# Kernel tuning notes

Measured on AMD Instinct MI355X. Metric: run time of the kernel, lower is better.

Reference implementation:

```python
import jax, jax.numpy as jnp
import numpy as np

V, D, H, L, T_MAX = 50257, 1024, 16, 12, 256
HS = D // H
B, T = 8, 256


def setup_inputs() -> dict:
    key = jax.random.key(0)
    ks = jax.random.split(key, 24)
    s = 0.02
    inp = {
        'idx': jax.random.randint(ks[0], (B, T), 0, V),
        'targets': jax.random.randint(ks[1], (B, T), 0, V),
        'tok_emb': jax.random.normal(ks[2], (V, D), jnp.float32) * s,
        'pos_emb': jax.random.normal(ks[3], (T_MAX, D), jnp.float32) * s,
        'Wq': jax.random.normal(ks[4], (L, H, D, HS), jnp.float32) / np.sqrt(D),
        'Wk': jax.random.normal(ks[5], (L, H, D, HS), jnp.float32) / np.sqrt(D),
        'Wv': jax.random.normal(ks[6], (L, H, D, HS), jnp.float32) / np.sqrt(D),
        'ln1_g': jnp.ones((L, D), jnp.float32),
        'ln1_b': jnp.zeros((L, D), jnp.float32),
        'ln2_g': jnp.ones((L, D), jnp.float32),
        'ln2_b': jnp.zeros((L, D), jnp.float32),
        'fc1_w': jax.random.normal(ks[7], (L, D, 4 * D), jnp.float32) / np.sqrt(D),
        'fc1_b': jnp.zeros((L, 4 * D), jnp.float32),
        'fc2_w': jax.random.normal(ks[8], (L, 4 * D, D), jnp.float32) / np.sqrt(4 * D),
        'fc2_b': jnp.zeros((L, D), jnp.float32),
        'lnf_g': jnp.ones((D,), jnp.float32),
        'lnf_b': jnp.zeros((D,), jnp.float32),
        'lm_w': jax.random.normal(ks[9], (D, V), jnp.float32) / np.sqrt(D),
        'lm_b': jnp.zeros((V,), jnp.float32),
    }
    return inp


def _layernorm(x, g, b, eps=1e-5):
    mu = jnp.mean(x, axis=-1, keepdims=True)
    var = jnp.var(x, axis=-1, keepdims=True)
    return (x - mu) * jax.lax.rsqrt(var + eps) * g + b


def reference(idx, targets, tok_emb, pos_emb, Wq, Wk, Wv, ln1_g, ln1_b, ln2_g, ln2_b,
              fc1_w, fc1_b, fc2_w, fc2_b, lnf_g, lnf_b, lm_w, lm_b):
    Bc, Tc = idx.shape
    x = tok_emb[idx] + pos_emb[:Tc]  # [B,T,D]
    causal = jnp.tril(jnp.ones((Tc, Tc), bool))
    scale = 1.0 / np.sqrt(HS)
    for l in range(L):
        h = _layernorm(x, ln1_g[l], ln1_b[l])
        q = jnp.einsum('btd,hds->bhts', h, Wq[l])
        k = jnp.einsum('btd,hds->bhts', h, Wk[l])
        v = jnp.einsum('btd,hds->bhts', h, Wv[l])
        scores = jnp.einsum('bhts,bhus->bhtu', q, k) * scale
        scores = jnp.where(causal, scores, -jnp.inf)
        attn = jax.nn.softmax(scores, axis=-1)
        o = jnp.einsum('bhtu,bhus->bhts', attn, v)  # [B,H,T,hs]
        o = o.transpose(0, 2, 1, 3).reshape(Bc, Tc, D)  # concat heads
        x = x + o  # no output projection in original
        h = _layernorm(x, ln2_g[l], ln2_b[l])
        ff = jax.nn.relu(h @ fc1_w[l] + fc1_b[l]) @ fc2_w[l] + fc2_b[l]
        x = x + ff
    x = _layernorm(x, lnf_g, lnf_b)
    logits = x @ lm_w + lm_b  # [B,T,V]
    logp = jax.nn.log_softmax(logits, axis=-1)
    nll = -jnp.take_along_axis(logp, targets[..., None], axis=-1)[..., 0]
    loss = jnp.mean(nll)
    return logits, loss
```

## Files before the change

kernel.cpp:

```cpp
#include <hip/hip_runtime.h>

#define T_SEQ 256
#define DMODEL 1024
#define NHEAD 16
#define HSZ 64
#define NLAYER 12
#define VOCAB 50257
#define NPAD 50304
#define FF 4096
#define MROWS 2048

using short8 = __attribute__((ext_vector_type(8))) short;
using f32x4  = __attribute__((ext_vector_type(4))) float;

__device__ __forceinline__ float bf2f(unsigned short u) {
    unsigned int x = ((unsigned int)u) << 16;
    return __builtin_bit_cast(float, x);
}
__device__ __forceinline__ unsigned short f2bf(float f) {
    unsigned int u = __builtin_bit_cast(unsigned int, f);
    unsigned int r = (u + 0x7fffu + ((u >> 16) & 1u)) >> 16;
    return (unsigned short)r;
}
__device__ __forceinline__ void async_copy16(const void* g, void* l) {
    __builtin_amdgcn_global_load_lds(
        (const __attribute__((address_space(1))) unsigned int*)g,
        (__attribute__((address_space(3))) unsigned int*)l, 16, 0, 0);
}

__device__ __forceinline__ void ln_tail(
    float4 v, const float* __restrict__ g, const float* __restrict__ b,
    int row, int tid, unsigned short* __restrict__ out)
{
    float s  = v.x + v.y + v.z + v.w;
    float ss = v.x * v.x + v.y * v.y + v.z * v.z + v.w * v.w;
    for (int o = 32; o > 0; o >>= 1) {
        s  += __shfl_down(s, o);
        ss += __shfl_down(ss, o);
    }
    __shared__ float ps[4], pss[4];
    int wave = tid >> 6, lane = tid & 63;
    if (lane == 0) { ps[wave] = s; pss[wave] = ss; }
    __syncthreads();
    float st  = ps[0] + ps[1] + ps[2] + ps[3];
    float sst = pss[0] + pss[1] + pss[2] + pss[3];
    float mu  = st * (1.0f / DMODEL);
    float var = sst * (1.0f / DMODEL) - mu * mu;
    float rstd = rsqrtf(var + 1e-5f);
    float4 gv = ((const float4*)g)[tid];
    float4 bv = ((const float4*)b)[tid];
    ushort4 o4;
    o4.x = f2bf((v.x - mu) * rstd * gv.x + bv.x);
    o4.y = f2bf((v.y - mu) * rstd * gv.y + bv.y);
    o4.z = f2bf((v.z - mu) * rstd * gv.z + bv.z);
    o4.w = f2bf((v.w - mu) * rstd * gv.w + bv.w);
    ((ushort4*)out)[(size_t)row * (DMODEL / 4) + tid] = o4;
}

__global__ __launch_bounds__(256) void embed_ln_kernel(
    const int* __restrict__ idx, const float* __restrict__ tok,
    const float* __restrict__ pos, const float* __restrict__ g,
    const float* __restrict__ b, float* __restrict__ x,
    unsigned short* __restrict__ h)
{
    int row = blockIdx.x, tid = threadIdx.x;
    int t = row & (T_SEQ - 1);
    int token = idx[row];
    float4 a = ((const float4*)(tok + (size_t)token * DMODEL))[tid];
    float4 p = ((const float4*)(pos + (size_t)t * DMODEL))[tid];
    float4 v;
    v.x = a.x + p.x; v.y = a.y + p.y; v.z = a.z + p.z; v.w = a.w + p.w;
    ((float4*)(x + (size_t)row * DMODEL))[tid] = v;
    ln_tail(v, g, b, row, tid, h);
}

__global__ __launch_bounds__(256) void ln_kernel(
    const float* __restrict__ x, const float* __restrict__ g,
    const float* __restrict__ b, unsigned short* __restrict__ out)
{
    int row = blockIdx.x, tid = threadIdx.x;
    float4 v = ((const float4*)(x + (size_t)row * DMODEL))[tid];
    ln_tail(v, g, b, row, tid, out);
}

__global__ __launch_bounds__(256) void fc2_merge_ln_kernel(
    const float* __restrict__ part, const float* __restrict__ bias,
    const float* __restrict__ g, const float* __restrict__ b,
    float* __restrict__ x, unsigned short* __restrict__ h)
{
    int row = blockIdx.x, tid = threadIdx.x;
    size_t o = (size_t)row * (DMODEL / 4) + tid;
    float4 p0 = ((const float4*)part)[o];
    float4 p1 = ((const float4*)part)[o + MROWS * (DMODEL / 4)];
    float4 bv = ((const float4*)bias)[tid];
    float4 v = ((float4*)x)[o];
    v.x += p0.x + p1.x + bv.x;
    v.y += p0.y + p1.y + bv.y;
    v.z += p0.z + p1.z + bv.z;
    v.w += p0.w + p1.w + bv.w;
    ((float4*)x)[o] = v;
    ln_tail(v, g, b, row, tid, h);
}

__global__ __launch_bounds__(256) void wtranspose_kernel(
    const float* __restrict__ in, unsigned short* __restrict__ out,
    int R, int C, int Cout, long in_l, long out_l)
{
    int lyr = blockIdx.z;
    in  += (size_t)lyr * in_l;
    out += (size_t)lyr * out_l;
    __shared__ float tile[32][33];
    int tx = threadIdx.x & 31, ty = threadIdx.x >> 5;
    int c0 = blockIdx.x * 32, r0 = blockIdx.y * 32;
    #pragma unroll
    for (int i = 0; i < 4; i++) {
        int r = r0 + ty + i * 8, c = c0 + tx;
        tile[ty + i * 8][tx] = (c < C) ? in[(size_t)r * C + c] : 0.f;
    }
    __syncthreads();
    #pragma unroll
    for (int i = 0; i < 4; i++) {
        int c = c0 + ty + i * 8, r = r0 + tx;
        if (c < Cout) out[(size_t)c * R + r] = f2bf(tile[tx][ty + i * 8]);
    }
}

__global__ __launch_bounds__(256) void qkvpack_kernel(
    const float* __restrict__ Wq, const float* __restrict__ Wk,
    const float* __restrict__ Wv, unsigned short* __restrict__ out,
    long w_l, long out_l)
{
    int z = blockIdx.z;
    int lyr = z / 48, r48 = z % 48;
    int seg = r48 >> 4, hh = r48 & 15;
    const float* W = (seg == 0 ? Wq : seg == 1 ? Wk : Wv)
                     + (size_t)lyr * w_l + (size_t)hh * DMODEL * HSZ;
    unsigned short* o = out + (size_t)lyr * out_l
                      + (size_t)(seg * 1024 + hh * 64) * DMODEL;
    __shared__ float tile[32][33];
    int tx = threadIdx.x & 31, ty = threadIdx.x >> 5;
    int d0 = blockIdx.x * 32, s0 = blockIdx.y * 32;
    #pragma unroll
    for (int i = 0; i < 4; i++)
        tile[ty + i * 8][tx] = W[(size_t)(d0 + ty + i * 8) * HSZ + s0 + tx];
    __syncthreads();
    #pragma unroll
    for (int i = 0; i < 4; i++)
        o[(size_t)(s0 + ty + i * 8) * DMODEL + d0 + tx] = f2bf(tile[tx][ty + i * 8]);
}

template<int MF, bool QKV, bool RELU, bool RES, bool CBF16>
__device__ __forceinline__ void gemm_core(
    const unsigned short* __restrict__ A, int lda,
    const unsigned short* __restrict__ Bt, int ldb,
    const float* __restrict__ bias,
    void* __restrict__ Cv, int ldc,
    const float* __restrict__ res, int ldr,
    int N, int K,
    unsigned short* __restrict__ vtout)
{
    constexpr int BM = MF * 32;
    __shared__ __align__(16) char As[2][BM * 128];
    __shared__ __align__(16) char Bs[2][128 * 128];
    int tid = threadIdx.x;
    int wave = tid >> 6, lane = tid & 63;
    int wr = wave >> 1, wc = wave & 1;
    int m0 = blockIdx.x * BM, n0 = blockIdx.y * 128;

    f32x4 acc[MF][4];
    #pragma unroll
    for (int m = 0; m < MF; m++)
        #pragma unroll
        for (int n = 0; n < 4; n++)
            acc[m][n] = (f32x4){0.f, 0.f, 0.f, 0.f};

    int ksw = (((lane & 7) ^ (lane >> 3)) << 4);
    int KT = K >> 6;

    auto stage = [&](int kt, int bi) {
        int k0 = kt << 6;
        #pragma unroll
        for (int j = 0; j < MF; j++) {
            int row = (wave * MF + j) * 8 + (lane >> 3);
            const char* src = (const char*)A + ((size_t)(m0 + row) * lda + k0) * 2 + ksw;
            async_copy16(src, As[bi] + (wave * MF + j) * 1024);
        }
        #pragma unroll
        for (int j = 0; j < 4; j++) {
            int nrow = (wave * 4 + j) * 8 + (lane >> 3);
            const char* src = (const char*)Bt + ((size_t)(n0 + nrow) * ldb + k0) * 2 + ksw;
            async_copy16(src, Bs[bi] + (wave * 4 + j) * 1024);
        }
    };

    stage(0, 0);
    __syncthreads();
    int cur = 0;
    for (int kt = 0; kt < KT; kt++) {
        if (kt + 1 < KT) stage(kt + 1, cur ^ 1);
        #pragma unroll
        for (int ks = 0; ks < 2; ks++) {
            int kb = ks * 64 + ((lane >> 4) << 4);
            short8 a[MF], b[4];
            #pragma unroll
            for (int m = 0; m < MF; m++) {
                int r = wr * (MF * 16) + m * 16 + (lane & 15);
                a[m] = *(const short8*)(const void*)(As[cur] + r * 128 + (kb ^ ((r & 7) << 4)));
            }
            #pragma unroll
            for (int n = 0; n < 4; n++) {
                int c = wc * 64 + n * 16 + (lane & 15);
                b[n] = *(const short8*)(const void*)(Bs[cur] + c * 128 + (kb ^ ((c & 7) << 4)));
            }
            #pragma unroll
            for (int m = 0; m < MF; m++)
                #pragma unroll
                for (int n = 0; n < 4; n++)
                    acc[m][n] = __builtin_amdgcn_mfma_f32_16x16x32_bf16(a[m], b[n], acc[m][n], 0, 0, 0);
        }
        __syncthreads();
        cur ^= 1;
    }
    #pragma unroll
    for (int m = 0; m < MF; m++) {
        int rowb = m0 + wr * (MF * 16) + m * 16 + ((lane >> 4) << 2);
        #pragma unroll
        for (int n = 0; n < 4; n++) {
            int col = n0 + wc * 64 + n * 16 + (lane & 15);
            if (col < N) {
                float bi = bias ? bias[col] : 0.f;
                #pragma unroll
                for (int r2 = 0; r2 < 4; r2++) {
                    float v = acc[m][n][r2] + bi;
                    if (RELU) v = fmaxf(v, 0.f);
                    int row = rowb + r2;
                    if (RES) v += res[(size_t)row * ldr + col];
                    if (QKV && col >= 2048) {
                        int hh = (col - 2048) >> 6, sdim = (col - 2048) & 63;
                        int bb = row >> 8, tt = row & 255;
                        vtout[((((size_t)bb * NHEAD + hh) * HSZ + sdim) * T_SEQ) + tt] = f2bf(v);
                    } else if (CBF16) {
                        ((unsigned short*)Cv)[(size_t)row * ldc + col] = f2bf(v);
                    } else {
                        ((float*)Cv)[(size_t)row * ldc + col] = v;
                    }
                }
            }
        }
    }
}

__global__ __launch_bounds__(256) void gemm_qkv(
    const unsigned short* __restrict__ A, const unsigned short* __restrict__ Bt,
    unsigned short* __restrict__ C, unsigned short* __restrict__ vtout)
{
    gemm_core<4, true, false, false, true>(
        A, DMODEL, Bt, DMODEL, nullptr, C, 3072, nullptr, 0, 3072, DMODEL, vtout);
}

__global__ __launch_bounds__(256) void gemm_fc1(
    const unsigned short* __restrict__ A, const unsigned short* __restrict__ Bt,
    const float* __restrict__ bias, unsigned short* __restrict__ C)
{
    gemm_core<4, false, true, false, true>(
        A, DMODEL, Bt, DMODEL, bias, C, FF, nullptr, 0, FF, DMODEL, nullptr);
}

__global__ __launch_bounds__(256) void gemm_fc2(
    const unsigned short* __restrict__ A, const unsigned short* __restrict__ Bt,
    float* __restrict__ part)
{
    int z = blockIdx.z;
    gemm_core<2, false, false, false, false>(
        A + z * 2048, FF, Bt + z * 2048, FF, nullptr,
        part + (size_t)z * MROWS * DMODEL, DMODEL, nullptr, 0,
        DMODEL, 2048, nullptr);
}

__global__ __launch_bounds__(256) void gemm_lm(
    const unsigned short* __restrict__ A, const unsigned short* __restrict__ Bt,
    const float* __restrict__ bias, float* __restrict__ C)
{
    gemm_core<4, false, false, false, false>(
        A, DMODEL, Bt, DMODEL, bias, C, VOCAB, nullptr, 0, VOCAB, DMODEL, nullptr);
}

__global__ __launch_bounds__(256) void attn_fused_kernel(
    const unsigned short* __restrict__ qkv, const unsigned short* __restrict__ vt,
    float* __restrict__ x)
{
    int qt = blockIdx.x, hh = blockIdx.y, b = blockIdx.z;
    int tid = threadIdx.x;
    int wave = tid >> 6, lane = tid & 63;
    int g = lane >> 4, q = lane & 15;

    __shared__ __align__(16) char Kb[2][8192];
    __shared__ __align__(16) char Vb[2][8192];
    __shared__ __align__(16) char Plds[4][2048];

    int qrow = b * T_SEQ + qt * 64 + wave * 16 + q;
    const char* qp = (const char*)qkv + ((size_t)qrow * 3072 + hh * HSZ) * 2;
    short8 qreg[2];
    qreg[0] = *(const short8*)(const void*)(qp + (g << 4));
    qreg[1] = *(const short8*)(const void*)(qp + 64 + (g << 4));

    char* Pw = Plds[wave];

    f32x4 oacc[4];
    #pragma unroll
    for (int f = 0; f < 4; f++) oacc[f] = (f32x4){0.f, 0.f, 0.f, 0.f};
    float m_run = -1e30f, l_run = 0.f;

    int srow = wave * 8 + (lane >> 3);
    int sbyte = ((lane & 7) << 4) ^ ((srow & 7) << 4);

    auto stage = [&](int kt, int bi) {
        #pragma unroll
        for (int c = 0; c < 2; c++) {
            int row = c * 32 + srow;
            const char* src = (const char*)qkv +
                ((size_t)(b * T_SEQ + kt * 64 + row) * 3072 + 1024 + hh * HSZ) * 2 + sbyte;
            async_copy16(src, Kb[bi] + c * 4096 + wave * 1024);
        }
        #pragma unroll
        for (int c = 0; c < 2; c++) {
            int row = c * 32 + srow;
            const char* src = (const char*)vt +
                (((size_t)(b * NHEAD + hh) * HSZ + row) * T_SEQ + kt * 64) * 2 + sbyte;
            async_copy16(src, Vb[bi] + c * 4096 + wave * 1024);
        }
    };

    stage(0, 0);
    for (int kt = 0; kt <= qt; kt++) {
        int bi = kt & 1;
        __syncthreads();
        if (kt < qt) stage(kt + 1, bi ^ 1);

        f32x4 sacc[4];
        #pragma unroll
        for (int f = 0; f < 4; f++) sacc[f] = (f32x4){0.f, 0.f, 0.f, 0.f};
        #pragma unroll
        for (int ks = 0; ks < 2; ks++) {
            int kb = ks * 64 + (g << 4);
            #pragma unroll
            for (int f = 0; f < 4; f++) {
                int u = f * 16 + q;
                short8 kf = *(const short8*)(const void*)(Kb[bi] + u * 128 + (kb ^ ((u & 7) << 4)));
                sacc[f] = __builtin_amdgcn_mfma_f32_16x16x32_bf16(kf, qreg[ks], sacc[f], 0, 0, 0);
            }
        }
        float sv[4][4];
        #pragma unroll
        for (int f = 0; f < 4; f++)
            #pragma unroll
            for (int r = 0; r < 4; r++) {
                float v = sacc[f][r] * 0.125f;
                if (kt == qt) {
                    int u_loc = f * 16 + g * 4 + r;
                    if (u_loc > wave * 16 + q) v = -1e30f;
                }
                sv[f][r] = v;
            }
        float pm = -1e30f;
        #pragma unroll
        for (int f = 0; f < 4; f++)
            #pragma unroll
            for (int r = 0; r < 4; r++) pm = fmaxf(pm, sv[f][r]);
        pm = fmaxf(pm, __shfl_xor(pm, 16));
        pm = fmaxf(pm, __shfl_xor(pm, 32));
        float mnew = fmaxf(m_run, pm);
        float corr = __expf(m_run - mnew);
        float p[4][4];
        float ls = 0.f;
        #pragma unroll
        for (int f = 0; f < 4; f++)
            #pragma unroll
            for (int r = 0; r < 4; r++) {
                p[f][r] = __expf(sv[f][r] - mnew);
                ls += p[f][r];
            }
        ls += __shfl_xor(ls, 16);
        ls += __shfl_xor(ls, 32);
        l_run = l_run * corr + ls;
        m_run = mnew;
        #pragma unroll
        for (int r = 0; r < 4; r++) {
            float cr = __shfl(corr, (lane & 48) | (g * 4 + r));
            #pragma unroll
            for (int f = 0; f < 4; f++) oacc[f][r] *= cr;
        }
        #pragma unroll
        for (int f = 0; f < 4; f++)
            #pragma unroll
            for (int rp = 0; rp < 2; rp++) {
                int ue = f * 16 + g * 4 + rp * 2;
                unsigned int pk = (unsigned int)f2bf(p[f][rp * 2])
                                | ((unsigned int)f2bf(p[f][rp * 2 + 1]) << 16);
                *(unsigned int*)(void*)(Pw + q * 128 + ((ue * 2) ^ ((q & 7) << 4))) = pk;
            }
        #pragma unroll
        for (int ks = 0; ks < 2; ks++) {
            int kb = ks * 64 + (g << 4);
            short8 pa = *(const short8*)(const void*)(Pw + q * 128 + (kb ^ ((q & 7) << 4)));
            #pragma unroll
            for (int f = 0; f < 4; f++) {
                int s = f * 16 + q;
                short8 vf = *(const short8*)(const void*)(Vb[bi] + s * 128 + (kb ^ ((s & 7) << 4)));
                oacc[f] = __builtin_amdgcn_mfma_f32_16x16x32_bf16(pa, vf, oacc[f], 0, 0, 0);
            }
        }
    }
    float inv = 1.0f / l_run;
    #pragma unroll
    for (int r = 0; r < 4; r++) {
        float ir = __shfl(inv, (lane & 48) | (g * 4 + r));
        int row_g = b * T_SEQ + qt * 64 + wave * 16 + g * 4 + r;
        #pragma unroll
        for (int f = 0; f < 4; f++) {
            size_t xi = (size_t)row_g * DMODEL + hh * HSZ + f * 16 + q;
            x[xi] += oacc[f][r] * ir;
        }
    }
}

__global__ __launch_bounds__(256) void loss1_kernel(
    const float* __restrict__ logits, const int* __restrict__ targets,
    float* __restrict__ nll)
{
    int r = blockIdx.x, tid = threadIdx.x;
    const float* row = logits + (size_t)r * VOCAB;
    const float4* row4 = (const float4*)row;
    float m = -3.4e38f, s = 0.f;
    for (int v = tid; v < VOCAB / 4; v += 256) {
        float4 x4 = row4[v];
        float lm = fmaxf(fmaxf(x4.x, x4.y), fmaxf(x4.z, x4.w));
        float nm = fmaxf(m, lm);
        s = s * __expf(m - nm) + __expf(x4.x - nm) + __expf(x4.y - nm)
          + __expf(x4.z - nm) + __expf(x4.w - nm);
        m = nm;
    }
    if (tid == 0) {
        float xv = row[VOCAB - 1];
        float nm = fmaxf(m, xv);
        s = s * __expf(m - nm) + __expf(xv - nm);
        m = nm;
    }
    __shared__ float ms[256], ssh[256];
    ms[tid] = m; ssh[tid] = s;
    __syncthreads();
    for (int o = 128; o > 0; o >>= 1) {
        if (tid < o) {
            float m1 = ms[tid], s1 = ssh[tid];
            float m2 = ms[tid + o], s2 = ssh[tid + o];
            float nm = fmaxf(m1, m2);
            ssh[tid] = s1 * __expf(m1 - nm) + s2 * __expf(m2 - nm);
            ms[tid] = nm;
        }
        __syncthreads();
    }
    if (tid == 0) nll[r] = logf(ssh[0]) + ms[0] - row[targets[r]];
}

__global__ __launch_bounds__(256) void loss2_kernel(
    const float* __restrict__ nll, float* __restrict__ out)
{
    int tid = threadIdx.x;
    float s = 0.f;
    for (int i = tid; i < MROWS; i += 256) s += nll[i];
    __shared__ float red[256];
    red[tid] = s;
    __syncthreads();
    for (int o = 128; o > 0; o >>= 1) {
        if (tid < o) red[tid] += red[tid + o];
        __syncthreads();
    }
    if (tid == 0) out[0] = red[0] * (1.0f / MROWS);
}

extern "C" void kernel_launch(void* const* d_in, const int* in_sizes, int n_in,
                              void* d_out, int out_size, void* d_ws, size_t ws_size,
                              hipStream_t stream)
{
    const int*   idx  = (const int*)d_in[0];
    const int*   tgt  = (const int*)d_in[1];
    const float* tok  = (const float*)d_in[2];
    const float* pos  = (const float*)d_in[3];
    const float* Wq   = (const float*)d_in[4];
    const float* Wk   = (const float*)d_in[5];
    const float* Wv   = (const float*)d_in[6];
    const float* ln1g = (const float*)d_in[7];
    const float* ln1b = (const float*)d_in[8];
    const float* ln2g = (const float*)d_in[9];
    const float* ln2b = (const float*)d_in[10];
    const float* fc1w = (const float*)d_in[11];
    const float* fc1b = (const float*)d_in[12];
    const float* fc2w = (const float*)d_in[13];
    const float* fc2b = (const float*)d_in[14];
    const float* lnfg = (const float*)d_in[15];
    const float* lnfb = (const float*)d_in[16];
    const float* lmw  = (const float*)d_in[17];
    const float* lmb  = (const float*)d_in[18];

    char* ws = (char*)d_ws;
    float*          x    = (float*)(ws + 0);
    unsigned short* h    = (unsigned short*)(ws + 8388608);
    unsigned short* qkv  = (unsigned short*)(ws + 12582912);
    unsigned short* vt   = (unsigned short*)(ws + 25165824);
    unsigned short* mid  = (unsigned short*)(ws + 29360128);
    float*          nll  = (float*)(ws + 46137344);
    float*          fc2p = (float*)(ws + 46145536);
    unsigned short* lmwt = (unsigned short*)(ws + 62922752);
    const size_t UP_NEED = 442769408ull;
    bool upfront = (ws_size >= UP_NEED);
    unsigned short* qkvt = (unsigned short*)(ws + 165945344);
    unsigned short* fc1t, * fc2t;
    long qkvt_l, fc1t_l, fc2t_l;
    if (upfront) {
        fc1t = (unsigned short*)(ws + 241442816);
        fc2t = (unsigned short*)(ws + 342106112);
        qkvt_l = 3072 * 1024; fc1t_l = (long)FF * 1024; fc2t_l = (long)1024 * FF;
    } else {
        fc1t = (unsigned short*)(ws + 172236800);
        fc2t = (unsigned short*)(ws + 180625408);
        qkvt_l = 0; fc1t_l = 0; fc2t_l = 0;
    }
    float* logits = (float*)d_out;
    float* lossp  = logits + (size_t)MROWS * VOCAB;

    const long WQKV_L = (long)NHEAD * DMODEL * HSZ;
    if (upfront) {
        qkvpack_kernel<<<dim3(32, 2, 48 * NLAYER), 256, 0, stream>>>(
            Wq, Wk, Wv, qkvt, WQKV_L, qkvt_l);
        wtranspose_kernel<<<dim3(128, 32, NLAYER), 256, 0, stream>>>(
            fc1w, fc1t, DMODEL, FF, FF, (long)DMODEL * FF, fc1t_l);
        wtranspose_kernel<<<dim3(32, 128, NLAYER), 256, 0, stream>>>(
            fc2w, fc2t, FF, DMODEL, DMODEL, (long)FF * DMODEL, fc2t_l);
    }
    wtranspose_kernel<<<dim3(1572, 32, 1), 256, 0, stream>>>(
        lmw, lmwt, DMODEL, VOCAB, NPAD, 0, 0);

    embed_ln_kernel<<<MROWS, 256, 0, stream>>>(idx, tok, pos, ln1g, ln1b, x, h);

    for (int l = 0; l < NLAYER; l++) {
        unsigned short* qkvt_p = qkvt + (size_t)l * qkvt_l;
        unsigned short* fc1t_p = fc1t + (size_t)l * fc1t_l;
        unsigned short* fc2t_p = fc2t + (size_t)l * fc2t_l;
        if (!upfront) {
            qkvpack_kernel<<<dim3(32, 2, 48), 256, 0, stream>>>(
                Wq + (size_t)l * WQKV_L, Wk + (size_t)l * WQKV_L,
                Wv + (size_t)l * WQKV_L, qkvt, WQKV_L, 0);
            wtranspose_kernel<<<dim3(128, 32, 1), 256, 0, stream>>>(
                fc1w + (size_t)l * DMODEL * FF, fc1t, DMODEL, FF, FF, 0, 0);
            wtranspose_kernel<<<dim3(32, 128, 1), 256, 0, stream>>>(
                fc2w + (size_t)l * FF * DMODEL, fc2t, FF, DMODEL, DMODEL, 0, 0);
        }
        gemm_qkv<<<dim3(16, 24), 256, 0, stream>>>(h, qkvt_p, qkv, vt);
        attn_fused_kernel<<<dim3(4, NHEAD, 8), 256, 0, stream>>>(qkv, vt, x);
        ln_kernel<<<MROWS, 256, 0, stream>>>(x, ln2g + l * DMODEL, ln2b + l * DMODEL, h);
        gemm_fc1<<<dim3(16, 32), 256, 0, stream>>>(h, fc1t_p, fc1b + (size_t)l * FF, mid);
        gemm_fc2<<<dim3(32, 8, 2), 256, 0, stream>>>(mid, fc2t_p, fc2p);
        const float* ng = (l < NLAYER - 1) ? ln1g + (l + 1) * DMODEL : lnfg;
        const float* nb = (l < NLAYER - 1) ? ln1b + (l + 1) * DMODEL : lnfb;
        fc2_merge_ln_kernel<<<MROWS, 256, 0, stream>>>(
            fc2p, fc2b + (size_t)l * DMODEL, ng, nb, x, h);
    }

    gemm_lm<<<dim3(16, 393), 256, 0, stream>>>(h, lmwt, lmb, logits);

    loss1_kernel<<<MROWS, 256, 0, stream>>>(logits, tgt, nll);
    loss2_kernel<<<1, 256, 0, stream>>>(nll, lossp);
}
```

Baseline: 2.257 ms.

## Drop GEMM double buffering and use 8-wave 256-row tiles for LM head

Replaces the double-buffered LDS staging in the shared GEMM core with a single buffer and two barriers per K step. This halves LDS use and may allow more blocks per CU. The LM-head GEMM now runs 512-thread blocks covering 256 rows, so each staged weight tile is reused across twice as many rows. In exchange, global loads no longer overlap with MFMA compute within a block, and all GEMMs pay an extra barrier per K step.

```diff
diff --git a/kernel.cpp b/kernel.cpp
--- a/kernel.cpp
+++ b/kernel.cpp
@@ -149,7 +149,7 @@
         o[(size_t)(s0 + ty + i * 8) * DMODEL + d0 + tx] = f2bf(tile[tx][ty + i * 8]);
 }
 
-template<int MF, bool QKV, bool RELU, bool RES, bool CBF16>
+template<int MF, int WAVES, bool QKV, bool RELU, bool RES, bool CBF16>
 __device__ __forceinline__ void gemm_core(
     const unsigned short* __restrict__ A, int lda,
     const unsigned short* __restrict__ Bt, int ldb,
@@ -159,9 +159,10 @@
     int N, int K,
     unsigned short* __restrict__ vtout)
 {
-    constexpr int BM = MF * 32;
-    __shared__ __align__(16) char As[2][BM * 128];
-    __shared__ __align__(16) char Bs[2][128 * 128];
+    constexpr int BM = (WAVES / 2) * MF * 16;
+    constexpr int BJ = 16 / WAVES;
+    __shared__ __align__(16) char As[BM * 128];
+    __shared__ __align__(16) char Bs[128 * 128];
     int tid = threadIdx.x;
     int wave = tid >> 6, lane = tid & 63;
     int wr = wave >> 1, wc = wave & 1;
@@ -176,28 +177,22 @@
 
     int ksw = (((lane & 7) ^ (lane >> 3)) << 4);
     int KT = K >> 6;
-
-    auto stage = [&](int kt, int bi) {
+    for (int kt = 0; kt < KT; kt++) {
         int k0 = kt << 6;
+        __syncthreads();
         #pragma unroll
         for (int j = 0; j < MF; j++) {
             int row = (wave * MF + j) * 8 + (lane >> 3);
             const char* src = (const char*)A + ((size_t)(m0 + row) * lda + k0) * 2 + ksw;
-            async_copy16(src, As[bi] + (wave * MF + j) * 1024);
-        }
-        #pragma unroll
-        for (int j = 0; j < 4; j++) {
-            int nrow = (wave * 4 + j) * 8 + (lane >> 3);
+            async_copy16(src, As + (wave * MF + j) * 1024);
+        }
+        #pragma unroll
+        for (int j = 0; j < BJ; j++) {
+            int nrow = (wave * BJ + j) * 8 + (lane >> 3);
             const char* src = (const char*)Bt + ((size_t)(n0 + nrow) * ldb + k0) * 2 + ksw;
-            async_copy16(src, Bs[bi] + (wave * 4 + j) * 1024);
-        }
-    };
-
-    stage(0, 0);
-    __syncthreads();
-    int cur = 0;
-    for (int kt = 0; kt < KT; kt++) {
-        if (kt + 1 < KT) stage(kt + 1, cur ^ 1);
+            async_copy16(src, Bs + (wave * BJ + j) * 1024);
+        }
+        __syncthreads();
         #pragma unroll
         for (int ks = 0; ks < 2; ks++) {
             int kb = ks * 64 + ((lane >> 4) << 4);
@@ -205,12 +200,12 @@
             #pragma unroll
             for (int m = 0; m < MF; m++) {
                 int r = wr * (MF * 16) + m * 16 + (lane & 15);
-                a[m] = *(const short8*)(const void*)(As[cur] + r * 128 + (kb ^ ((r & 7) << 4)));
+                a[m] = *(const short8*)(const void*)(As + r * 128 + (kb ^ ((r & 7) << 4)));
             }
             #pragma unroll
             for (int n = 0; n < 4; n++) {
                 int c = wc * 64 + n * 16 + (lane & 15);
-                b[n] = *(const short8*)(const void*)(Bs[cur] + c * 128 + (kb ^ ((c & 7) << 4)));
+                b[n] = *(const short8*)(const void*)(Bs + c * 128 + (kb ^ ((c & 7) << 4)));
             }
             #pragma unroll
             for (int m = 0; m < MF; m++)
@@ -218,8 +213,6 @@
                 for (int n = 0; n < 4; n++)
                     acc[m][n] = __builtin_amdgcn_mfma_f32_16x16x32_bf16(a[m], b[n], acc[m][n], 0, 0, 0);
         }
-        __syncthreads();
-        cur ^= 1;
     }
     #pragma unroll
     for (int m = 0; m < MF; m++) {
@@ -254,7 +247,7 @@
     const unsigned short* __restrict__ A, const unsigned short* __restrict__ Bt,
     unsigned short* __restrict__ C, unsigned short* __restrict__ vtout)
 {
-    gemm_core<4, true, false, false, true>(
+    gemm_core<4, 4, true, false, false, true>(
         A, DMODEL, Bt, DMODEL, nullptr, C, 3072, nullptr, 0, 3072, DMODEL, vtout);
 }
 
@@ -262,7 +255,7 @@
     const unsigned short* __restrict__ A, const unsigned short* __restrict__ Bt,
     const float* __restrict__ bias, unsigned short* __restrict__ C)
 {
-    gemm_core<4, false, true, false, true>(
+    gemm_core<4, 4, false, true, false, true>(
         A, DMODEL, Bt, DMODEL, bias, C, FF, nullptr, 0, FF, DMODEL, nullptr);
 }
 
@@ -271,17 +264,17 @@
     float* __restrict__ part)
 {
     int z = blockIdx.z;
-    gemm_core<2, false, false, false, false>(
+    gemm_core<2, 4, false, false, false, false>(
         A + z * 2048, FF, Bt + z * 2048, FF, nullptr,
         part + (size_t)z * MROWS * DMODEL, DMODEL, nullptr, 0,
         DMODEL, 2048, nullptr);
 }
 
-__global__ __launch_bounds__(256) void gemm_lm(
+__global__ __launch_bounds__(512) void gemm_lm(
     const unsigned short* __restrict__ A, const unsigned short* __restrict__ Bt,
     const float* __restrict__ bias, float* __restrict__ C)
 {
-    gemm_core<4, false, false, false, false>(
+    gemm_core<4, 8, false, false, false, false>(
         A, DMODEL, Bt, DMODEL, bias, C, VOCAB, nullptr, 0, VOCAB, DMODEL, nullptr);
 }
 
@@ -566,7 +559,7 @@
             fc2p, fc2b + (size_t)l * DMODEL, ng, nb, x, h);
     }
 
-    gemm_lm<<<dim3(16, 393), 256, 0, stream>>>(h, lmwt, lmb, logits);
+    gemm_lm<<<dim3(8, 393), 512, 0, stream>>>(h, lmwt, lmb, logits);
 
     loss1_kernel<<<MROWS, 256, 0, stream>>>(logits, tgt, nll);
     loss2_kernel<<<1, 256, 0, stream>>>(nll, lossp);
```

Measured after the change: 2.122 ms. -6.0%, faster.
